# Performance work log

Measured on AMD Instinct MI355X. Metric: run time of the kernel, lower is better.

## Reference

```python
import jax, jax.numpy as jnp
import numpy as np

DIM = 512
NUM_HEADS = 8
DIM_HEAD = 64
EPS = 1e-8
ROPE_THETA = 10000.0


def rms_norm(x, gamma):
    # F.normalize(x, dim=-1, p=2, eps) * sqrt(dim) * gamma
    norm = jnp.sqrt(jnp.sum(x * x, axis=-1, keepdims=True))
    x = x / jnp.maximum(norm, EPS)
    return x * (DIM ** 0.5) * gamma


def apply_rope(x):
    # x: [b, h, n, d], interleaved-pair RoPE (rotary-embedding-torch style)
    n, d = x.shape[-2], x.shape[-1]
    inv_freq = 1.0 / (ROPE_THETA ** (jnp.arange(0, d, 2, dtype=jnp.float32) / d))
    freqs = jnp.arange(n, dtype=jnp.float32)[:, None] * inv_freq[None, :]  # [n, d/2]
    freqs = jnp.repeat(freqs, 2, axis=-1)  # [n, d]
    cos, sin = jnp.cos(freqs), jnp.sin(freqs)
    x1 = x[..., ::2]
    x2 = x[..., 1::2]
    rot = jnp.stack((-x2, x1), axis=-1).reshape(x.shape)
    return x * cos + rot * sin


def setup_inputs() -> dict:
    key = jax.random.key(0)
    k1, k2, k3, k4 = jax.random.split(key, 4)
    b, n = 4, 2048
    dim_inner = NUM_HEADS * DIM_HEAD
    x = jax.random.normal(k1, (b, n, DIM), dtype=jnp.float32)
    gamma = jnp.ones((DIM,), dtype=jnp.float32)
    w_qkv = jax.random.normal(k2, (DIM, 3 * dim_inner), dtype=jnp.float32) * (DIM ** -0.5)
    w_out = jax.random.normal(k3, (dim_inner, DIM), dtype=jnp.float32) * (dim_inner ** -0.5)
    return {"x": x, "gamma": gamma, "w_qkv": w_qkv, "w_out": w_out}


def reference(x, gamma, w_qkv, w_out):
    b, n, _ = x.shape
    h, d = NUM_HEADS, DIM_HEAD
    xn = rms_norm(x, gamma)
    qkv = xn @ w_qkv  # [b, n, 3*h*d]
    qkv = qkv.reshape(b, n, 3, h, d)
    q = jnp.transpose(qkv[:, :, 0], (0, 2, 1, 3))  # [b, h, n, d]
    k = jnp.transpose(qkv[:, :, 1], (0, 2, 1, 3))
    v = jnp.transpose(qkv[:, :, 2], (0, 2, 1, 3))
    q = apply_rope(q)
    k = apply_rope(k)
    scale = d ** -0.5
    attn = jnp.einsum('bhnd,bhmd->bhnm', q, k) * scale
    attn = jax.nn.softmax(attn, axis=-1)
    out = jnp.einsum('bhnm,bhmd->bhnd', attn, v)
    out = jnp.transpose(out, (0, 2, 1, 3)).reshape(b, n, h * d)
    return out @ w_out
```

## Files before the change

kernel.cpp:

```cpp
#include <hip/hip_runtime.h>
#include <hip/hip_bf16.h>
#include <cmath>

#define B_SZ 4
#define N_SEQ 2048
#define DIM 512
#define NH 8
#define DH 64
#define QKV_N 1536
#define ROWS (B_SZ * N_SEQ)

typedef __bf16 bf16x8 __attribute__((ext_vector_type(8)));
typedef __bf16 bf16x4 __attribute__((ext_vector_type(4)));
typedef float  f32x4  __attribute__((ext_vector_type(4)));

#define GLOAD_LDS16(gp, lp)                                                     \
    __builtin_amdgcn_global_load_lds(                                           \
        (const __attribute__((address_space(1))) void*)(gp),                    \
        (__attribute__((address_space(3))) void*)(lp), 16, 0, 0)

#define MFMA_BF16 __builtin_amdgcn_mfma_f32_16x16x32_bf16

__device__ __forceinline__ void tcast_tile(const float* __restrict__ W,
                                           __bf16* __restrict__ Wt,
                                           int K, int N, int n0, int k0, int t,
                                           float (*Ls)[68]) {
    const int tx = t & 15, ty = t >> 4;
    #pragma unroll
    for (int i = 0; i < 4; i++) {
        int k = ty + i * 16;
        float4 v = *(const float4*)&W[(size_t)(k0 + k) * N + n0 + tx * 4];
        *(float4*)&Ls[k][tx * 4] = v;
    }
    __syncthreads();
    const int nrow = t >> 2, seg = (t & 3) * 16;
    bf16x8 o0, o1;
    #pragma unroll
    for (int j = 0; j < 8; j++) o0[j] = (__bf16)Ls[seg + j][nrow];
    #pragma unroll
    for (int j = 0; j < 8; j++) o1[j] = (__bf16)Ls[seg + 8 + j][nrow];
    *(bf16x8*)&Wt[(size_t)(n0 + nrow) * K + k0 + seg]     = o0;
    *(bf16x8*)&Wt[(size_t)(n0 + nrow) * K + k0 + seg + 8] = o1;
}

__global__ __launch_bounds__(256) void prelude_kernel(const float* __restrict__ x,
                                                      const float* __restrict__ gamma,
                                                      const float* __restrict__ w_qkv,
                                                      const float* __restrict__ w_out,
                                                      __bf16* __restrict__ A,
                                                      __bf16* __restrict__ Wqkvt,
                                                      __bf16* __restrict__ Woutt) {
    __shared__ float Ls[64][68];
    const int bx = blockIdx.x, t = threadIdx.x;
    if (bx < 2048) {
        const int row  = bx * 4 + (t >> 6);
        const int lane = t & 63;
        const float4* xr = (const float4*)(x + (size_t)row * DIM);
        float4 a = xr[lane];
        float4 b = xr[lane + 64];
        float ss = a.x*a.x + a.y*a.y + a.z*a.z + a.w*a.w
                 + b.x*b.x + b.y*b.y + b.z*b.z + b.w*b.w;
        #pragma unroll
        for (int off = 32; off > 0; off >>= 1) ss += __shfl_xor(ss, off, 64);
        float s = 22.62741699796952f / fmaxf(sqrtf(ss), 1e-8f);
        const float4* gr = (const float4*)gamma;
        float4 g1 = gr[lane], g2 = gr[lane + 64];
        bf16x4 o1 = { (__bf16)(a.x*g1.x*s), (__bf16)(a.y*g1.y*s),
                      (__bf16)(a.z*g1.z*s), (__bf16)(a.w*g1.w*s) };
        bf16x4 o2 = { (__bf16)(b.x*g2.x*s), (__bf16)(b.y*g2.y*s),
                      (__bf16)(b.z*g2.z*s), (__bf16)(b.w*g2.w*s) };
        *(bf16x4*)(A + (size_t)row * DIM + lane * 4)       = o1;
        *(bf16x4*)(A + (size_t)row * DIM + 256 + lane * 4) = o2;
    } else {
        const int idx = bx - 2048;
        const int k0 = (idx >> 5) * 64, c = idx & 31;
        if (c < 24) tcast_tile(w_qkv, Wqkvt, DIM, QKV_N, c * 64, k0, t, Ls);
        else        tcast_tile(w_out, Woutt, DIM, DIM, (c - 24) * 64, k0, t, Ls);
    }
}

template <int N, typename OutT>
__global__ __launch_bounds__(256) void gemm_bf16_kernel(const __bf16* __restrict__ A,
                                                        const __bf16* __restrict__ Bt,
                                                        OutT* __restrict__ C) {
    __shared__ __bf16 As[128 * 32];
    __shared__ __bf16 Bs[128 * 32];
    const int t = threadIdx.x;
    const int lane = t & 63;
    const int w = t >> 6;
    const int l16 = lane & 15, quad = lane >> 4;
    const int wr = w >> 1, wc = w & 1;
    const int row0 = blockIdx.y * 128, col0 = blockIdx.x * 128;

    f32x4 acc[4][4] = {};

    const int r0a = t >> 2,         ks0 = (t & 3) * 8;
    const int r1a = (t + 256) >> 2, ks1 = (t & 3) * 8;

    for (int kt = 0; kt < DIM; kt += 32) {
        __syncthreads();
        GLOAD_LDS16(A  + (size_t)(row0 + r0a) * DIM + kt + ks0, As + t * 8);
        GLOAD_LDS16(A  + (size_t)(row0 + r1a) * DIM + kt + ks1, As + (t + 256) * 8);
        GLOAD_LDS16(Bt + (size_t)(col0 + r0a) * DIM + kt + ks0, Bs + t * 8);
        GLOAD_LDS16(Bt + (size_t)(col0 + r1a) * DIM + kt + ks1, Bs + (t + 256) * 8);
        __syncthreads();
        bf16x8 af[4], bfr[4];
        #pragma unroll
        for (int mi = 0; mi < 4; mi++)
            af[mi] = *(const bf16x8*)(As + (wr * 64 + mi * 16 + l16) * 32 + quad * 8);
        #pragma unroll
        for (int ni = 0; ni < 4; ni++)
            bfr[ni] = *(const bf16x8*)(Bs + (wc * 64 + ni * 16 + l16) * 32 + quad * 8);
        #pragma unroll
        for (int mi = 0; mi < 4; mi++)
            #pragma unroll
            for (int ni = 0; ni < 4; ni++)
                acc[mi][ni] = MFMA_BF16(af[mi], bfr[ni], acc[mi][ni], 0, 0, 0);
    }
    #pragma unroll
    for (int mi = 0; mi < 4; mi++) {
        #pragma unroll
        for (int ni = 0; ni < 4; ni++) {
            #pragma unroll
            for (int r = 0; r < 4; r++) {
                int m = row0 + wr * 64 + mi * 16 + quad * 4 + r;
                int n = col0 + wc * 64 + ni * 16 + l16;
                if constexpr (sizeof(OutT) == 4) {
                    C[(size_t)m * N + n] = acc[mi][ni][r];
                } else {
                    C[(size_t)m * N + n] = (__bf16)acc[mi][ni][r];
                }
            }
        }
    }
}

__global__ __launch_bounds__(256) void gemm_out_kernel(const __bf16* __restrict__ A,
                                                       const __bf16* __restrict__ Bt,
                                                       float* __restrict__ C) {
    __shared__ __bf16 As[64 * 32];
    __shared__ __bf16 Bs[128 * 32];
    const int t = threadIdx.x;
    const int lane = t & 63;
    const int w = t >> 6;
    const int l16 = lane & 15, quad = lane >> 4;
    const int wr = w >> 1, wc = w & 1;
    const int row0 = blockIdx.y * 64, col0 = blockIdx.x * 128;

    f32x4 acc[2][4] = {};

    const int r0a = t >> 2, ks0 = (t & 3) * 8;
    const int r1a = (t + 256) >> 2;

    for (int kt = 0; kt < DIM; kt += 32) {
        __syncthreads();
        GLOAD_LDS16(A  + (size_t)(row0 + r0a) * DIM + kt + ks0, As + t * 8);
        GLOAD_LDS16(Bt + (size_t)(col0 + r0a) * DIM + kt + ks0, Bs + t * 8);
        GLOAD_LDS16(Bt + (size_t)(col0 + r1a) * DIM + kt + ks0, Bs + (t + 256) * 8);
        __syncthreads();
        bf16x8 af[2], bfr[4];
        #pragma unroll
        for (int mi = 0; mi < 2; mi++)
            af[mi] = *(const bf16x8*)(As + (wr * 32 + mi * 16 + l16) * 32 + quad * 8);
        #pragma unroll
        for (int ni = 0; ni < 4; ni++)
            bfr[ni] = *(const bf16x8*)(Bs + (wc * 64 + ni * 16 + l16) * 32 + quad * 8);
        #pragma unroll
        for (int mi = 0; mi < 2; mi++)
            #pragma unroll
            for (int ni = 0; ni < 4; ni++)
                acc[mi][ni] = MFMA_BF16(af[mi], bfr[ni], acc[mi][ni], 0, 0, 0);
    }
    #pragma unroll
    for (int mi = 0; mi < 2; mi++)
        #pragma unroll
        for (int ni = 0; ni < 4; ni++)
            #pragma unroll
            for (int r = 0; r < 4; r++) {
                int m = row0 + wr * 32 + mi * 16 + quad * 4 + r;
                int n = col0 + wc * 64 + ni * 16 + l16;
                C[(size_t)m * 512 + n] = acc[mi][ni][r];
            }
}

__global__ __launch_bounds__(256) void prep_kernel(const __bf16* __restrict__ qkvb,
                                                   __bf16* __restrict__ Qb,
                                                   __bf16* __restrict__ Kf,
                                                   __bf16* __restrict__ Vf) {
    const int bx = blockIdx.x;
    const int nt = bx & 31;
    const int bh = bx >> 5;
    const int b  = bh >> 3;
    const int h  = bh & 7;
    const int t  = threadIdx.x;
    const float QSCALE = 0.18033688011112042f;

    {
        const int r  = t >> 2;
        const int d0 = (t & 3) << 4;
        const int pos = nt * 64 + r;
        const __bf16* qp = qkvb + (size_t)(b * N_SEQ + pos) * QKV_N + h * DH + d0;

        union Pack { __bf16 h[16]; uint4 u[2]; };
        Pack qi, ki, qo, ko;
        qi.u[0] = ((const uint4*)qp)[0];         qi.u[1] = ((const uint4*)qp)[1];
        ki.u[0] = ((const uint4*)(qp + 512))[0]; ki.u[1] = ((const uint4*)(qp + 512))[1];

        #pragma unroll
        for (int i = 0; i < 8; i++) {
            int p = (d0 >> 1) + i;
            float inv = exp2f(-0.41524101186092028f * (float)p);
            float ang = (float)pos * inv;
            float sn, cs;
            sincosf(ang, &sn, &cs);
            float qe = (float)qi.h[2*i], qd = (float)qi.h[2*i+1];
            float ke = (float)ki.h[2*i], kd = (float)ki.h[2*i+1];
            qo.h[2*i]   = (__bf16)(QSCALE * (qe * cs - qd * sn));
            qo.h[2*i+1] = (__bf16)(QSCALE * (qd * cs + qe * sn));
            ko.h[2*i]   = (__bf16)(ke * cs - kd * sn);
            ko.h[2*i+1] = (__bf16)(kd * cs + ke * sn);
        }
        uint4* qd_ = (uint4*)(Qb + ((size_t)bh * N_SEQ + pos) * DH + d0);
        qd_[0] = qo.u[0]; qd_[1] = qo.u[1];
        const int group = r >> 4, kl = r & 15;
        const int c = d0 >> 5, quad = (d0 & 31) >> 3;
        __bf16* kdst = Kf + ((size_t)bh * 32 + nt) * 4096
                          + (group * 2 + c) * 512 + (quad * 16 + kl) * 8;
        *(uint4*)kdst         = ko.u[0];
        *(uint4*)(kdst + 128) = ko.u[1];
    }

    {
        const int w = t >> 6, lane = t & 63;
        union PackV { __bf16 h[16]; unsigned long long q[4]; };
        PackV v;
        #pragma unroll
        for (int j = 0; j < 16; j++) {
            int row = nt * 64 + w * 16 + j;
            v.h[j] = qkvb[(size_t)(b * N_SEQ + row) * QKV_N + 1024 + h * DH + lane];
        }
        const int ng = lane >> 4, vl = lane & 15;
        __bf16* vdst = Vf + ((size_t)bh * 32 + nt) * 4096
                          + (ng * 2 + (w >> 1)) * 512 + vl * 8 + (w & 1) * 4;
        #pragma unroll
        for (int q = 0; q < 4; q++)
            *(unsigned long long*)(vdst + q * 128) = v.q[q];
    }
}

__global__ __launch_bounds__(256, 2) void attn_mfma_kernel(const __bf16* __restrict__ Qb,
                                                           const __bf16* __restrict__ Kf,
                                                           const __bf16* __restrict__ Vf,
                                                           __bf16* __restrict__ attn) {
    __shared__ __bf16 kv[2][16384];

    const int t    = threadIdx.x;
    const int w    = t >> 6;
    const int lane = t & 63;
    const int l16  = lane & 15;
    const int quad = lane >> 4;

    const int bx = blockIdx.x;
    const int bh = bx & 31;
    const int qc = bx >> 5;
    const int b  = bh >> 3;
    const int h  = bh & 7;

    const int qrow = qc * 128 + w * 32;
    const __bf16* Qh = Qb + ((size_t)bh * N_SEQ + qrow) * DH;
    const __bf16* Kt = Kf + (size_t)bh * 32 * 4096;
    const __bf16* Vt = Vf + (size_t)bh * 32 * 4096;

    bf16x8 qa[2][2];
    #pragma unroll
    for (int f = 0; f < 2; f++) {
        qa[f][0] = *(const bf16x8*)(Qh + (size_t)(f * 16 + l16) * DH + quad * 8);
        qa[f][1] = *(const bf16x8*)(Qh + (size_t)(f * 16 + l16) * DH + 32 + quad * 8);
    }

    bf16x8 ones;
    #pragma unroll
    for (int i = 0; i < 8; i++) ones[i] = (__bf16)1.0f;

    f32x4 O[2][4] = {};
    f32x4 L[2] = {};

    auto dma_tile = [&](int tt, int bb) {
        const __bf16* kss = Kt + (size_t)tt * 8192;
        const __bf16* vss = Vt + (size_t)tt * 8192;
        #pragma unroll
        for (int seg = 0; seg < 2; seg++) {
            GLOAD_LDS16(kss + seg * 4096 + w * 512 + lane * 8,
                        &kv[bb][seg * 4096 + w * 512 + lane * 8]);
            GLOAD_LDS16(kss + seg * 4096 + (w + 4) * 512 + lane * 8,
                        &kv[bb][seg * 4096 + (w + 4) * 512 + lane * 8]);
            GLOAD_LDS16(vss + seg * 4096 + w * 512 + lane * 8,
                        &kv[bb][8192 + seg * 4096 + w * 512 + lane * 8]);
            GLOAD_LDS16(vss + seg * 4096 + (w + 4) * 512 + lane * 8,
                        &kv[bb][8192 + seg * 4096 + (w + 4) * 512 + lane * 8]);
        }
    };

    dma_tile(0, 0);
    for (int tt = 0; tt < 16; tt++) {
        const int cur = tt & 1;
        __syncthreads();
        if (tt + 1 < 16) {
            dma_tile(tt + 1, cur ^ 1);
            asm volatile("s_waitcnt vmcnt(8)" ::: "memory");
        } else {
            asm volatile("s_waitcnt vmcnt(0)" ::: "memory");
        }
        __syncthreads();

        #pragma unroll
        for (int hh = 0; hh < 2; hh++) {
            const __bf16* kb = kv[cur] + hh * 4096;
            const __bf16* vb = kv[cur] + 8192 + hh * 4096;

            bf16x8 kf[4][2];
            #pragma unroll
            for (int g = 0; g < 4; g++)
                #pragma unroll
                for (int c = 0; c < 2; c++)
                    kf[g][c] = *(const bf16x8*)(kb + (g * 2 + c) * 512 + lane * 8);
            bf16x8 vf[4][2];
            #pragma unroll
            for (int n = 0; n < 4; n++)
                #pragma unroll
                for (int kc = 0; kc < 2; kc++)
                    vf[n][kc] = *(const bf16x8*)(vb + (n * 2 + kc) * 512 + lane * 8);

            #pragma unroll
            for (int f = 0; f < 2; f++) {
                f32x4 S[4];
                #pragma unroll
                for (int g = 0; g < 4; g++) {
                    f32x4 z = {0, 0, 0, 0};
                    z = MFMA_BF16(kf[g][0], qa[f][0], z, 0, 0, 0);
                    z = MFMA_BF16(kf[g][1], qa[f][1], z, 0, 0, 0);
                    S[g] = z;
                }
                bf16x8 pa0, pa1;
                #pragma unroll
                for (int j = 0; j < 8; j++) {
                    pa0[j] = (__bf16)__builtin_amdgcn_exp2f(S[(j >> 2)][j & 3]);
                    pa1[j] = (__bf16)__builtin_amdgcn_exp2f(S[2 + (j >> 2)][j & 3]);
                }
                #pragma unroll
                for (int n = 0; n < 4; n++) {
                    O[f][n] = MFMA_BF16(pa0, vf[n][0], O[f][n], 0, 0, 0);
                    O[f][n] = MFMA_BF16(pa1, vf[n][1], O[f][n], 0, 0, 0);
                }
                L[f] = MFMA_BF16(pa0, ones, L[f], 0, 0, 0);
                L[f] = MFMA_BF16(pa1, ones, L[f], 0, 0, 0);
            }
        }
    }

    #pragma unroll
    for (int f = 0; f < 2; f++) {
        float inv[4];
        #pragma unroll
        for (int r = 0; r < 4; r++) inv[r] = 1.0f / L[f][r];
        #pragma unroll
        for (int n = 0; n < 4; n++)
            #pragma unroll
            for (int r = 0; r < 4; r++) {
                size_t row = (size_t)(b * N_SEQ + qrow + f * 16 + quad * 4 + r);
                attn[row * 512 + h * DH + n * 16 + l16] = (__bf16)(O[f][n][r] * inv[r]);
            }
    }
}

extern "C" void kernel_launch(void* const* d_in, const int* in_sizes, int n_in,
                              void* d_out, int out_size, void* d_ws, size_t ws_size,
                              hipStream_t stream) {
    const float* x     = (const float*)d_in[0];
    const float* gamma = (const float*)d_in[1];
    const float* w_qkv = (const float*)d_in[2];
    const float* w_out = (const float*)d_in[3];
    float* out = (float*)d_out;

    __bf16* Abf   = (__bf16*)d_ws;
    __bf16* Wqkvt = Abf + (size_t)ROWS * DIM;
    __bf16* Woutt = Wqkvt + (size_t)QKV_N * DIM;
    __bf16* qkvb  = Woutt + (size_t)DIM * DIM;
    __bf16* attnb = qkvb;
    __bf16* Qb    = qkvb + (size_t)ROWS * QKV_N;
    __bf16* Kf    = Qb + (size_t)NH * B_SZ * N_SEQ * DH;
    __bf16* Vf    = Kf + (size_t)NH * B_SZ * N_SEQ * DH;

    prelude_kernel<<<2304, 256, 0, stream>>>(x, gamma, w_qkv, w_out,
                                             Abf, Wqkvt, Woutt);
    gemm_bf16_kernel<QKV_N, __bf16><<<dim3(QKV_N / 128, ROWS / 128), 256, 0, stream>>>(
        Abf, Wqkvt, qkvb);
    prep_kernel<<<1024, 256, 0, stream>>>(qkvb, Qb, Kf, Vf);
    attn_mfma_kernel<<<512, 256, 0, stream>>>(Qb, Kf, Vf, attnb);
    gemm_out_kernel<<<dim3(4, 128), 256, 0, stream>>>(attnb, Woutt, out);
}
```

Before: 153.0 us.

## Shrink attention tiles to 16 query rows per wave and 64-key K/V tiles

The attention kernel now gives each wave 16 query rows instead of 32 and streams K/V in 64-key tiles instead of 128, which halves the LDS buffer. Launch bounds rise to 4 blocks per SM and the grid doubles to 1024 blocks. The aim is more occupancy and more blocks to hide latency and fill the 256 CUs. In exchange, each K/V fragment loaded from LDS is reused across half as many query rows, so LDS and global traffic per FLOP doubles, and there are twice as many barrier iterations.

Result: slower. 156.8 us (+2.5%).

```diff
diff --git a/kernel.cpp b/kernel.cpp
--- a/kernel.cpp
+++ b/kernel.cpp
@@ -248,11 +248,11 @@
     }
 }
 
-__global__ __launch_bounds__(256, 2) void attn_mfma_kernel(const __bf16* __restrict__ Qb,
+__global__ __launch_bounds__(256, 4) void attn_mfma_kernel(const __bf16* __restrict__ Qb,
                                                            const __bf16* __restrict__ Kf,
                                                            const __bf16* __restrict__ Vf,
                                                            __bf16* __restrict__ attn) {
-    __shared__ __bf16 kv[2][16384];
+    __shared__ __bf16 kv[2][8192];
 
     const int t    = threadIdx.x;
     const int w    = t >> 6;
@@ -266,111 +266,94 @@
     const int b  = bh >> 3;
     const int h  = bh & 7;
 
-    const int qrow = qc * 128 + w * 32;
+    const int qrow = qc * 64 + w * 16;
     const __bf16* Qh = Qb + ((size_t)bh * N_SEQ + qrow) * DH;
     const __bf16* Kt = Kf + (size_t)bh * 32 * 4096;
     const __bf16* Vt = Vf + (size_t)bh * 32 * 4096;
 
-    bf16x8 qa[2][2];
-    #pragma unroll
-    for (int f = 0; f < 2; f++) {
-        qa[f][0] = *(const bf16x8*)(Qh + (size_t)(f * 16 + l16) * DH + quad * 8);
-        qa[f][1] = *(const bf16x8*)(Qh + (size_t)(f * 16 + l16) * DH + 32 + quad * 8);
-    }
+    bf16x8 qa[2];
+    qa[0] = *(const bf16x8*)(Qh + (size_t)l16 * DH + quad * 8);
+    qa[1] = *(const bf16x8*)(Qh + (size_t)l16 * DH + 32 + quad * 8);
 
     bf16x8 ones;
     #pragma unroll
     for (int i = 0; i < 8; i++) ones[i] = (__bf16)1.0f;
 
-    f32x4 O[2][4] = {};
-    f32x4 L[2] = {};
+    f32x4 O[4] = {};
+    f32x4 L = {};
 
     auto dma_tile = [&](int tt, int bb) {
-        const __bf16* kss = Kt + (size_t)tt * 8192;
-        const __bf16* vss = Vt + (size_t)tt * 8192;
-        #pragma unroll
-        for (int seg = 0; seg < 2; seg++) {
-            GLOAD_LDS16(kss + seg * 4096 + w * 512 + lane * 8,
-                        &kv[bb][seg * 4096 + w * 512 + lane * 8]);
-            GLOAD_LDS16(kss + seg * 4096 + (w + 4) * 512 + lane * 8,
-                        &kv[bb][seg * 4096 + (w + 4) * 512 + lane * 8]);
-            GLOAD_LDS16(vss + seg * 4096 + w * 512 + lane * 8,
-                        &kv[bb][8192 + seg * 4096 + w * 512 + lane * 8]);
-            GLOAD_LDS16(vss + seg * 4096 + (w + 4) * 512 + lane * 8,
-                        &kv[bb][8192 + seg * 4096 + (w + 4) * 512 + lane * 8]);
-        }
+        const __bf16* kss = Kt + (size_t)tt * 4096;
+        const __bf16* vss = Vt + (size_t)tt * 4096;
+        GLOAD_LDS16(kss + t * 8,        &kv[bb][t * 8]);
+        GLOAD_LDS16(kss + 2048 + t * 8, &kv[bb][2048 + t * 8]);
+        GLOAD_LDS16(vss + t * 8,        &kv[bb][4096 + t * 8]);
+        GLOAD_LDS16(vss + 2048 + t * 8, &kv[bb][4096 + 2048 + t * 8]);
     };
 
     dma_tile(0, 0);
-    for (int tt = 0; tt < 16; tt++) {
+    for (int tt = 0; tt < 32; tt++) {
         const int cur = tt & 1;
         __syncthreads();
-        if (tt + 1 < 16) {
+        if (tt + 1 < 32) {
             dma_tile(tt + 1, cur ^ 1);
-            asm volatile("s_waitcnt vmcnt(8)" ::: "memory");
+            asm volatile("s_waitcnt vmcnt(4)" ::: "memory");
         } else {
             asm volatile("s_waitcnt vmcnt(0)" ::: "memory");
         }
         __syncthreads();
 
-        #pragma unroll
-        for (int hh = 0; hh < 2; hh++) {
-            const __bf16* kb = kv[cur] + hh * 4096;
-            const __bf16* vb = kv[cur] + 8192 + hh * 4096;
-
-            bf16x8 kf[4][2];
-            #pragma unroll
-            for (int g = 0; g < 4; g++)
-                #pragma unroll
-                for (int c = 0; c < 2; c++)
-                    kf[g][c] = *(const bf16x8*)(kb + (g * 2 + c) * 512 + lane * 8);
-            bf16x8 vf[4][2];
-            #pragma unroll
-            for (int n = 0; n < 4; n++)
-                #pragma unroll
-                for (int kc = 0; kc < 2; kc++)
-                    vf[n][kc] = *(const bf16x8*)(vb + (n * 2 + kc) * 512 + lane * 8);
-
-            #pragma unroll
-            for (int f = 0; f < 2; f++) {
-                f32x4 S[4];
-                #pragma unroll
-                for (int g = 0; g < 4; g++) {
-                    f32x4 z = {0, 0, 0, 0};
-                    z = MFMA_BF16(kf[g][0], qa[f][0], z, 0, 0, 0);
-                    z = MFMA_BF16(kf[g][1], qa[f][1], z, 0, 0, 0);
-                    S[g] = z;
-                }
-                bf16x8 pa0, pa1;
-                #pragma unroll
-                for (int j = 0; j < 8; j++) {
-                    pa0[j] = (__bf16)__builtin_amdgcn_exp2f(S[(j >> 2)][j & 3]);
-                    pa1[j] = (__bf16)__builtin_amdgcn_exp2f(S[2 + (j >> 2)][j & 3]);
-                }
-                #pragma unroll
-                for (int n = 0; n < 4; n++) {
-                    O[f][n] = MFMA_BF16(pa0, vf[n][0], O[f][n], 0, 0, 0);
-                    O[f][n] = MFMA_BF16(pa1, vf[n][1], O[f][n], 0, 0, 0);
-                }
-                L[f] = MFMA_BF16(pa0, ones, L[f], 0, 0, 0);
-                L[f] = MFMA_BF16(pa1, ones, L[f], 0, 0, 0);
-            }
-        }
-    }
-
-    #pragma unroll
-    for (int f = 0; f < 2; f++) {
-        float inv[4];
-        #pragma unroll
-        for (int r = 0; r < 4; r++) inv[r] = 1.0f / L[f][r];
+        const __bf16* kb = kv[cur];
+        const __bf16* vb = kv[cur] + 4096;
+
+        bf16x8 kf[4][2];
+        #pragma unroll
+        for (int g = 0; g < 4; g++)
+            #pragma unroll
+            for (int c = 0; c < 2; c++)
+                kf[g][c] = *(const bf16x8*)(kb + (g * 2 + c) * 512 + lane * 8);
+
+        f32x4 S[4];
+        #pragma unroll
+        for (int g = 0; g < 4; g++) {
+            f32x4 z = {0, 0, 0, 0};
+            z = MFMA_BF16(kf[g][0], qa[0], z, 0, 0, 0);
+            z = MFMA_BF16(kf[g][1], qa[1], z, 0, 0, 0);
+            S[g] = z;
+        }
+        bf16x8 pa0, pa1;
+        #pragma unroll
+        for (int j = 0; j < 8; j++) {
+            pa0[j] = (__bf16)__builtin_amdgcn_exp2f(S[(j >> 2)][j & 3]);
+            pa1[j] = (__bf16)__builtin_amdgcn_exp2f(S[2 + (j >> 2)][j & 3]);
+        }
+
+        bf16x8 vf[4][2];
         #pragma unroll
         for (int n = 0; n < 4; n++)
             #pragma unroll
-            for (int r = 0; r < 4; r++) {
-                size_t row = (size_t)(b * N_SEQ + qrow + f * 16 + quad * 4 + r);
-                attn[row * 512 + h * DH + n * 16 + l16] = (__bf16)(O[f][n][r] * inv[r]);
-            }
-    }
+            for (int kc = 0; kc < 2; kc++)
+                vf[n][kc] = *(const bf16x8*)(vb + (n * 2 + kc) * 512 + lane * 8);
+
+        #pragma unroll
+        for (int n = 0; n < 4; n++) {
+            O[n] = MFMA_BF16(pa0, vf[n][0], O[n], 0, 0, 0);
+            O[n] = MFMA_BF16(pa1, vf[n][1], O[n], 0, 0, 0);
+        }
+        L = MFMA_BF16(pa0, ones, L, 0, 0, 0);
+        L = MFMA_BF16(pa1, ones, L, 0, 0, 0);
+    }
+
+    float inv[4];
+    #pragma unroll
+    for (int r = 0; r < 4; r++) inv[r] = 1.0f / L[r];
+    #pragma unroll
+    for (int n = 0; n < 4; n++)
+        #pragma unroll
+        for (int r = 0; r < 4; r++) {
+            size_t row = (size_t)(b * N_SEQ + qrow + quad * 4 + r);
+            attn[row * 512 + h * DH + n * 16 + l16] = (__bf16)(O[n][r] * inv[r]);
+        }
 }
 
 extern "C" void kernel_launch(void* const* d_in, const int* in_sizes, int n_in,
@@ -396,6 +379,6 @@
     gemm_bf16_kernel<QKV_N, __bf16><<<dim3(QKV_N / 128, ROWS / 128), 256, 0, stream>>>(
         Abf, Wqkvt, qkvb);
     prep_kernel<<<1024, 256, 0, stream>>>(qkvb, Qb, Kf, Vf);
-    attn_mfma_kernel<<<512, 256, 0, stream>>>(Qb, Kf, Vf, attnb);
+    attn_mfma_kernel<<<1024, 256, 0, stream>>>(Qb, Kf, Vf, attnb);
     gemm_out_kernel<<<dim3(4, 128), 256, 0, stream>>>(attnb, Woutt, out);
 }
```

## Split attention key range across wave pairs with LDS reduction of partial outputs

Applied to the files above, without the earlier changes.

Each wave now handles 64 query rows instead of 32, and the two waves in a pair each process half of every key/value tile (split-K). Partial O and L accumulators are combined through LDS at the end. The aim is to halve the LDS reads of K/V fragments per wave relative to MFMA work and raise per-wave arithmetic intensity. The cost is doubled accumulator and P register usage, which may push against the 2-blocks-per-CU launch bound and spill, plus an extra LDS reduction and barrier at the end.

Measured after the change: 153.1 us. About the same (+0.1%).

```diff
diff --git a/kernel.cpp b/kernel.cpp
--- a/kernel.cpp
+++ b/kernel.cpp
@@ -252,13 +252,15 @@
                                                            const __bf16* __restrict__ Kf,
                                                            const __bf16* __restrict__ Vf,
                                                            __bf16* __restrict__ attn) {
-    __shared__ __bf16 kv[2][16384];
+    __shared__ __bf16 kv[2][2][8192];
 
     const int t    = threadIdx.x;
     const int w    = t >> 6;
     const int lane = t & 63;
     const int l16  = lane & 15;
     const int quad = lane >> 4;
+    const int qh   = w >> 1;
+    const int kp   = w & 1;
 
     const int bx = blockIdx.x;
     const int bh = bx & 31;
@@ -266,14 +268,14 @@
     const int b  = bh >> 3;
     const int h  = bh & 7;
 
-    const int qrow = qc * 128 + w * 32;
-    const __bf16* Qh = Qb + ((size_t)bh * N_SEQ + qrow) * DH;
+    const int qrow0 = qc * 128 + qh * 64;
+    const __bf16* Qh = Qb + ((size_t)bh * N_SEQ + qrow0) * DH;
     const __bf16* Kt = Kf + (size_t)bh * 32 * 4096;
     const __bf16* Vt = Vf + (size_t)bh * 32 * 4096;
 
-    bf16x8 qa[2][2];
-    #pragma unroll
-    for (int f = 0; f < 2; f++) {
+    bf16x8 qa[4][2];
+    #pragma unroll
+    for (int f = 0; f < 4; f++) {
         qa[f][0] = *(const bf16x8*)(Qh + (size_t)(f * 16 + l16) * DH + quad * 8);
         qa[f][1] = *(const bf16x8*)(Qh + (size_t)(f * 16 + l16) * DH + 32 + quad * 8);
     }
@@ -282,94 +284,116 @@
     #pragma unroll
     for (int i = 0; i < 8; i++) ones[i] = (__bf16)1.0f;
 
-    f32x4 O[2][4] = {};
-    f32x4 L[2] = {};
-
-    auto dma_tile = [&](int tt, int bb) {
-        const __bf16* kss = Kt + (size_t)tt * 8192;
-        const __bf16* vss = Vt + (size_t)tt * 8192;
-        #pragma unroll
-        for (int seg = 0; seg < 2; seg++) {
-            GLOAD_LDS16(kss + seg * 4096 + w * 512 + lane * 8,
-                        &kv[bb][seg * 4096 + w * 512 + lane * 8]);
-            GLOAD_LDS16(kss + seg * 4096 + (w + 4) * 512 + lane * 8,
-                        &kv[bb][seg * 4096 + (w + 4) * 512 + lane * 8]);
-            GLOAD_LDS16(vss + seg * 4096 + w * 512 + lane * 8,
-                        &kv[bb][8192 + seg * 4096 + w * 512 + lane * 8]);
-            GLOAD_LDS16(vss + seg * 4096 + (w + 4) * 512 + lane * 8,
-                        &kv[bb][8192 + seg * 4096 + (w + 4) * 512 + lane * 8]);
-        }
+    f32x4 O[4][4] = {};
+    f32x4 L[4] = {};
+
+    auto dma_tile = [&](int tidx, int p, int pp) {
+        const __bf16* kss = Kt + (size_t)tidx * 4096;
+        const __bf16* vss = Vt + (size_t)tidx * 4096;
+        __bf16* dst = &kv[p][pp][0];
+        GLOAD_LDS16(kss + t * 8,        dst + t * 8);
+        GLOAD_LDS16(kss + 2048 + t * 8, dst + 2048 + t * 8);
+        GLOAD_LDS16(vss + t * 8,        dst + 4096 + t * 8);
+        GLOAD_LDS16(vss + 2048 + t * 8, dst + 4096 + 2048 + t * 8);
     };
 
-    dma_tile(0, 0);
-    for (int tt = 0; tt < 16; tt++) {
-        const int cur = tt & 1;
-        __syncthreads();
-        if (tt + 1 < 16) {
-            dma_tile(tt + 1, cur ^ 1);
+    dma_tile(0, 0, 0);
+    dma_tile(1, 1, 0);
+    for (int i = 0; i < 16; i++) {
+        const int cur = i & 1;
+        __syncthreads();
+        if (i + 1 < 16) {
+            dma_tile(2 * (i + 1),     0, cur ^ 1);
+            dma_tile(2 * (i + 1) + 1, 1, cur ^ 1);
             asm volatile("s_waitcnt vmcnt(8)" ::: "memory");
         } else {
             asm volatile("s_waitcnt vmcnt(0)" ::: "memory");
         }
         __syncthreads();
 
-        #pragma unroll
-        for (int hh = 0; hh < 2; hh++) {
-            const __bf16* kb = kv[cur] + hh * 4096;
-            const __bf16* vb = kv[cur] + 8192 + hh * 4096;
-
-            bf16x8 kf[4][2];
-            #pragma unroll
-            for (int g = 0; g < 4; g++)
-                #pragma unroll
-                for (int c = 0; c < 2; c++)
-                    kf[g][c] = *(const bf16x8*)(kb + (g * 2 + c) * 512 + lane * 8);
-            bf16x8 vf[4][2];
+        const __bf16* kb = &kv[kp][cur][0];
+        const __bf16* vb = &kv[kp][cur][4096];
+
+        bf16x8 kf[4][2];
+        #pragma unroll
+        for (int g = 0; g < 4; g++)
+            #pragma unroll
+            for (int c = 0; c < 2; c++)
+                kf[g][c] = *(const bf16x8*)(kb + (g * 2 + c) * 512 + lane * 8);
+
+        bf16x8 pa[4][2];
+        #pragma unroll
+        for (int f = 0; f < 4; f++) {
+            f32x4 S[4];
+            #pragma unroll
+            for (int g = 0; g < 4; g++) {
+                f32x4 z = {0, 0, 0, 0};
+                z = MFMA_BF16(kf[g][0], qa[f][0], z, 0, 0, 0);
+                z = MFMA_BF16(kf[g][1], qa[f][1], z, 0, 0, 0);
+                S[g] = z;
+            }
+            #pragma unroll
+            for (int j = 0; j < 8; j++) {
+                pa[f][0][j] = (__bf16)__builtin_amdgcn_exp2f(S[(j >> 2)][j & 3]);
+                pa[f][1][j] = (__bf16)__builtin_amdgcn_exp2f(S[2 + (j >> 2)][j & 3]);
+            }
+        }
+
+        bf16x8 vf[4][2];
+        #pragma unroll
+        for (int n = 0; n < 4; n++)
+            #pragma unroll
+            for (int kc = 0; kc < 2; kc++)
+                vf[n][kc] = *(const bf16x8*)(vb + (n * 2 + kc) * 512 + lane * 8);
+
+        #pragma unroll
+        for (int f = 0; f < 4; f++) {
+            #pragma unroll
+            for (int n = 0; n < 4; n++) {
+                O[f][n] = MFMA_BF16(pa[f][0], vf[n][0], O[f][n], 0, 0, 0);
+                O[f][n] = MFMA_BF16(pa[f][1], vf[n][1], O[f][n], 0, 0, 0);
+            }
+            L[f] = MFMA_BF16(pa[f][0], ones, L[f], 0, 0, 0);
+            L[f] = MFMA_BF16(pa[f][1], ones, L[f], 0, 0, 0);
+        }
+    }
+
+    __syncthreads();
+    float* reds = (float*)&kv[0][0][0];
+    float* myO = reds + (size_t)(qh * 64 + lane) * 68;
+    float* myL = reds + 128 * 68 + (size_t)(qh * 64 + lane) * 20;
+    if (kp == 1) {
+        #pragma unroll
+        for (int f = 0; f < 4; f++) {
+            #pragma unroll
+            for (int n = 0; n < 4; n++)
+                *(f32x4*)(myO + (f * 4 + n) * 4) = O[f][n];
+            *(f32x4*)(myL + f * 4) = L[f];
+        }
+    }
+    __syncthreads();
+    if (kp == 0) {
+        #pragma unroll
+        for (int f = 0; f < 4; f++) {
+            #pragma unroll
+            for (int n = 0; n < 4; n++)
+                O[f][n] += *(const f32x4*)(myO + (f * 4 + n) * 4);
+            L[f] += *(const f32x4*)(myL + f * 4);
+        }
+        #pragma unroll
+        for (int f = 0; f < 4; f++) {
+            float inv[4];
+            #pragma unroll
+            for (int r = 0; r < 4; r++) inv[r] = 1.0f / L[f][r];
             #pragma unroll
             for (int n = 0; n < 4; n++)
                 #pragma unroll
-                for (int kc = 0; kc < 2; kc++)
-                    vf[n][kc] = *(const bf16x8*)(vb + (n * 2 + kc) * 512 + lane * 8);
-
-            #pragma unroll
-            for (int f = 0; f < 2; f++) {
-                f32x4 S[4];
-                #pragma unroll
-                for (int g = 0; g < 4; g++) {
-                    f32x4 z = {0, 0, 0, 0};
-                    z = MFMA_BF16(kf[g][0], qa[f][0], z, 0, 0, 0);
-                    z = MFMA_BF16(kf[g][1], qa[f][1], z, 0, 0, 0);
-                    S[g] = z;
+                for (int r = 0; r < 4; r++) {
+                    size_t row = (size_t)(b * N_SEQ + qrow0 + f * 16 + quad * 4 + r);
+                    attn[row * 512 + h * DH + n * 16 + l16] =
+                        (__bf16)(O[f][n][r] * inv[r]);
                 }
-                bf16x8 pa0, pa1;
-                #pragma unroll
-                for (int j = 0; j < 8; j++) {
-                    pa0[j] = (__bf16)__builtin_amdgcn_exp2f(S[(j >> 2)][j & 3]);
-                    pa1[j] = (__bf16)__builtin_amdgcn_exp2f(S[2 + (j >> 2)][j & 3]);
-                }
-                #pragma unroll
-                for (int n = 0; n < 4; n++) {
-                    O[f][n] = MFMA_BF16(pa0, vf[n][0], O[f][n], 0, 0, 0);
-                    O[f][n] = MFMA_BF16(pa1, vf[n][1], O[f][n], 0, 0, 0);
-                }
-                L[f] = MFMA_BF16(pa0, ones, L[f], 0, 0, 0);
-                L[f] = MFMA_BF16(pa1, ones, L[f], 0, 0, 0);
-            }
-        }
-    }
-
-    #pragma unroll
-    for (int f = 0; f < 2; f++) {
-        float inv[4];
-        #pragma unroll
-        for (int r = 0; r < 4; r++) inv[r] = 1.0f / L[f][r];
-        #pragma unroll
-        for (int n = 0; n < 4; n++)
-            #pragma unroll
-            for (int r = 0; r < 4; r++) {
-                size_t row = (size_t)(b * N_SEQ + qrow + f * 16 + quad * 4 + r);
-                attn[row * 512 + h * DH + n * 16 + l16] = (__bf16)(O[f][n][r] * inv[r]);
-            }
+        }
     }
 }
 
```
